# Kernel optimization log

Hardware: AMD Instinct MI355X
Metric: run time of the kernel (lower is better)

Reference implementation:

```python
import jax, jax.numpy as jnp
import numpy as np

B, N, F, D = 32, 1024, 128, 128
SCALE = 0.5


def setup_inputs() -> dict:
    key = jax.random.key(0)
    ks = jax.random.split(key, 8)
    atom_query = jax.random.normal(ks[0], (B, N, F), dtype=jnp.float32)
    # binary validity mask (some atoms padded out), shape [B, N, 1]
    mask = (jax.random.uniform(ks[1], (B, N, 1)) < 0.9).astype(jnp.float32)
    s = 1.0 / np.sqrt(F)
    Wq = jax.random.normal(ks[2], (F, D), dtype=jnp.float32) * s
    Wk = jax.random.normal(ks[3], (F, D), dtype=jnp.float32) * s
    Wv = jax.random.normal(ks[4], (F, D), dtype=jnp.float32) * s
    bq = jnp.zeros((D,), jnp.float32)
    bk = jnp.zeros((D,), jnp.float32)
    bv = jnp.zeros((D,), jnp.float32)
    return {"atom_query": atom_query, "mask": mask,
            "Wq": Wq, "bq": bq, "Wk": Wk, "bk": bk, "Wv": Wv, "bv": bv}


def reference(atom_query, mask, Wq, bq, Wk, bk, Wv, bv):
    # projections
    q = atom_query @ Wq + bq            # [B,N,D]
    k = atom_query @ Wk + bk            # [B,N,D]
    v = atom_query @ Wv + bv            # [B,N,D]
    n = q.shape[1]
    dk = (q.shape[-1] ** (-SCALE)) / n  # python float scalar
    q = q * jnp.float32(dk)
    # pairwise energy [B,N,N]
    energy = jnp.einsum('bqd,bkd->bqk', q, k)
    energy = energy * mask              # mask query rows ([B,N,1] broadcast)
    idx = jnp.arange(n)
    energy = energy.at[:, idx, idx].set(0.0)  # remove self-interaction (diag)
    # aggregate attention per query atom [B,N,1]
    agg = jnp.sum(energy, axis=-1, keepdims=True) * mask
    # euclidean normalize along atom axis (tf.linalg.normalize, axis=1)
    nrm = jnp.sqrt(jnp.sum(agg * agg, axis=1, keepdims=True))
    agg = agg / nrm
    agg = agg + (1.0 - mask) * (-1e9)
    attn = jax.nn.softmax(agg, axis=1)  # softmax over atom (query) axis
    # weighted sum of values -> [B,D]
    context = jnp.sum(mask * (attn * v), axis=1)
    return attn, context
```

## Files before the change

### kernel.cpp

```cpp
#include <hip/hip_runtime.h>

#define B_ 32
#define N_ 1024
#define DK_CONST 8.631674575031098e-05f

typedef unsigned short u16;
typedef __attribute__((ext_vector_type(8))) short short8;
typedef __attribute__((ext_vector_type(4))) float floatx4;

__device__ __forceinline__ u16 f2b(float x) {
    union { float f; unsigned u; } v; v.f = x;
    unsigned u = v.u;
    return (u16)((u + 0x7FFFu + ((u >> 16) & 1u)) >> 16);
}
__device__ __forceinline__ float b2f(u16 h) {
    union { unsigned u; float f; } v; v.u = ((unsigned)h) << 16;
    return v.f;
}

__global__ __launch_bounds__(256) void k1_prep(const float* __restrict__ aq,
                                               const float* __restrict__ Wq,
                                               const float* __restrict__ Wk,
                                               float* __restrict__ colsumPart,
                                               u16* __restrict__ WqT,
                                               u16* __restrict__ WkT) {
    __shared__ float cspart[256][4];
    __shared__ float tr[128][132];
    int t = threadIdx.x;
    int blk = blockIdx.x;
    if (blk < 256) {
        const float4* aq4 = (const float4*)(aq + (size_t)blk * 16384);
        float c0 = 0.f, c1 = 0.f, c2 = 0.f, c3 = 0.f;
        for (int j = 0; j < 16; ++j) {
            float4 v = aq4[t + 256 * j];
            c0 += v.x; c1 += v.y; c2 += v.z; c3 += v.w;
        }
        cspart[t][0] = c0; cspart[t][1] = c1; cspart[t][2] = c2; cspart[t][3] = c3;
        __syncthreads();
        if (t < 128) {
            int c4i = t >> 2, comp = t & 3;
            float s = 0.f;
            for (int h = 0; h < 8; ++h) s += cspart[h * 32 + c4i][comp];
            colsumPart[blk * 128 + t] = s;
        }
    } else {
        const float* W = (blk == 256) ? Wq : Wk;
        u16* WT = (blk == 256) ? WqT : WkT;
        const float4* W4 = (const float4*)W;
        for (int j = 0; j < 16; ++j) {
            int idx = t + 256 * j;
            int f  = idx >> 5;
            int d4 = (idx & 31) * 4;
            float4 v = W4[idx];
            *((float4*)&tr[f][d4]) = v;
        }
        __syncthreads();
        for (int j = 0; j < 16; ++j) {
            int idx = t + 256 * j;
            int d = idx >> 5;
            int c = idx & 31;
            ushort4 o;
            o.x = f2b(tr[4 * c][d]);
            o.y = f2b(tr[4 * c + 1][d]);
            o.z = f2b(tr[4 * c + 2][d]);
            o.w = f2b(tr[4 * c + 3][d]);
            ((ushort4*)WT)[d * 32 + c] = o;
        }
    }
}

__global__ __launch_bounds__(256, 1) void k2_agg(const float* __restrict__ aq,
                                                 const float* __restrict__ mask,
                                                 const float* __restrict__ Wk,
                                                 const float* __restrict__ bq,
                                                 const float* __restrict__ bk,
                                                 const u16* __restrict__ WqT,
                                                 const u16* __restrict__ WkT,
                                                 const float* __restrict__ colsumPart,
                                                 float* __restrict__ agg,
                                                 float* __restrict__ ssqPart) {
    __shared__ __align__(16) u16 aqT[128][136];
    __shared__ __align__(16) u16 wqS[128][136];
    __shared__ __align__(16) u16 wkS[128][136];
    __shared__ float qpart[2][128];
    __shared__ float Ksum_s[128];
    __shared__ float bq_s[128], bk_s[128];
    __shared__ float Ss[128];
    __shared__ float red[256];

    int t = threadIdx.x;
    int tile = blockIdx.x;
    int b = tile >> 3;

    const float4* aq4 = (const float4*)(aq + (size_t)tile * 16384);
    for (int j = 0; j < 16; ++j) {
        int idx = t + 256 * j;
        int row = idx >> 5;
        int c4  = idx & 31;
        float4 v = aq4[idx];
        ushort4 bb;
        bb.x = f2b(v.x); bb.y = f2b(v.y); bb.z = f2b(v.z); bb.w = f2b(v.w);
        *((ushort4*)&aqT[row][c4 * 4]) = bb;
    }
    for (int j = 0; j < 16; ++j) {
        int idx = t + 256 * j;
        int row = idx >> 5;
        int c4  = idx & 31;
        ushort4 q4 = ((const ushort4*)WqT)[idx];
        *((ushort4*)&wqS[row][c4 * 4]) = q4;
        ushort4 k4 = ((const ushort4*)WkT)[idx];
        *((ushort4*)&wkS[row][c4 * 4]) = k4;
    }
    if (t < 128) {
        float s = 0.f;
        for (int h = 0; h < 8; ++h) s += colsumPart[(b * 8 + h) * 128 + t];
        Ss[t] = s;
        bq_s[t] = bq[t];
        bk_s[t] = bk[t];
    }
    __syncthreads();
    if (t < 128) {
        float kd = 1024.0f * bk_s[t];
        for (int f = 0; f < 128; ++f) kd += Ss[f] * Wk[f * 128 + t];
        Ksum_s[t] = kd;
    }
    __syncthreads();

    int w = t >> 6;
    int lane = t & 63;
    int wr   = (w >> 1) * 64;
    int wcol = (w & 1) * 64;
    int lm = lane & 15;
    int lq = lane >> 4;

    floatx4 acc1[4][4], acc2[4][4];
    for (int i = 0; i < 4; ++i)
        for (int j = 0; j < 4; ++j) {
            acc1[i][j] = (floatx4){0.f, 0.f, 0.f, 0.f};
            acc2[i][j] = (floatx4){0.f, 0.f, 0.f, 0.f};
        }

    for (int ks = 0; ks < 4; ++ks) {
        int k0 = ks * 32 + lq * 8;
        short8 afr[4], bq_f[4], bk_f[4];
        for (int i = 0; i < 4; ++i) {
            afr[i]  = *(const short8*)&aqT[wr + i * 16 + lm][k0];
            bq_f[i] = *(const short8*)&wqS[wcol + i * 16 + lm][k0];
            bk_f[i] = *(const short8*)&wkS[wcol + i * 16 + lm][k0];
        }
        for (int i = 0; i < 4; ++i)
            for (int j = 0; j < 4; ++j) {
                acc1[i][j] = __builtin_amdgcn_mfma_f32_16x16x32_bf16(afr[i], bq_f[j], acc1[i][j], 0, 0, 0);
                acc2[i][j] = __builtin_amdgcn_mfma_f32_16x16x32_bf16(afr[i], bk_f[j], acc2[i][j], 0, 0, 0);
            }
    }

    for (int mi = 0; mi < 4; ++mi) {
        for (int r = 0; r < 4; ++r) {
            int row = wr + mi * 16 + lq * 4 + r;
            float s = 0.f;
            for (int nj = 0; nj < 4; ++nj) {
                int col = wcol + nj * 16 + lm;
                float qv = acc1[mi][nj][r] + bq_s[col];
                float kv = Ksum_s[col] - acc2[mi][nj][r] - bk_s[col];
                s += qv * kv;
            }
            s += __shfl_xor(s, 1);
            s += __shfl_xor(s, 2);
            s += __shfl_xor(s, 4);
            s += __shfl_xor(s, 8);
            if (lm == 0) qpart[w & 1][row] = s;
        }
    }
    __syncthreads();
    float a2 = 0.f;
    if (t < 128) {
        int atom = tile * 128 + t;
        float a = mask[atom] * DK_CONST * (qpart[0][t] + qpart[1][t]);
        agg[atom] = a;
        a2 = a * a;
    }
    red[t] = a2;
    __syncthreads();
    for (int st = 128; st > 0; st >>= 1) { if (t < st) red[t] += red[t + st]; __syncthreads(); }
    if (t == 0) ssqPart[tile] = red[0];
}

__global__ __launch_bounds__(1024) void k3_fin(const float* __restrict__ aq,
                                               const float* __restrict__ mask,
                                               const float* __restrict__ Wv,
                                               const float* __restrict__ bv,
                                               const float* __restrict__ agg,
                                               const float* __restrict__ ssqPart,
                                               float* __restrict__ attnOut,
                                               float* __restrict__ ctxOut) {
    __shared__ float el[1024];
    __shared__ float red[1024];
    __shared__ float accs[32][128];
    __shared__ float pvec[128];
    __shared__ float sc0;
    int b = blockIdx.x, t = threadIdx.x;

    if (t == 0) {
        float ss = 0.f;
        for (int h = 0; h < 8; ++h) ss += ssqPart[b * 8 + h];
        sc0 = 1.0f / sqrtf(ss);
    }
    __syncthreads();
    float invn = sc0;
    int atom = b * N_ + t;
    float a = agg[atom];
    float m = mask[atom];
    float e = (m > 0.5f) ? expf(a * invn) : 0.f;
    el[t] = e;
    red[t] = e;
    __syncthreads();
    for (int st = 512; st > 0; st >>= 1) {
        if (t < st) red[t] += red[t + st];
        __syncthreads();
    }
    float invE = 1.0f / red[0];
    attnOut[atom] = e * invE;

    int f4 = t & 31, g = t >> 5;
    const float4* aqb4 = (const float4*)(aq + (size_t)b * N_ * 128);
    float4 acc; acc.x = acc.y = acc.z = acc.w = 0.f;
    for (int i = g; i < 1024; i += 32) {
        float4 v = aqb4[i * 32 + f4];
        float wgt = el[i];
        acc.x += wgt * v.x; acc.y += wgt * v.y; acc.z += wgt * v.z; acc.w += wgt * v.w;
    }
    *((float4*)&accs[g][f4 * 4]) = acc;
    __syncthreads();
    if (t < 128) {
        float p = 0.f;
        for (int gg = 0; gg < 32; ++gg) p += accs[gg][t];
        pvec[t] = p;
    }
    __syncthreads();
    if (t < 128) {
        float c = 0.f;
        for (int f = 0; f < 128; ++f) c += pvec[f] * Wv[f * 128 + t];
        ctxOut[b * 128 + t] = c * invE + bv[t];
    }
}

extern "C" void kernel_launch(void* const* d_in, const int* in_sizes, int n_in,
                              void* d_out, int out_size, void* d_ws, size_t ws_size,
                              hipStream_t stream) {
    const float* aq   = (const float*)d_in[0];
    const float* mask = (const float*)d_in[1];
    const float* Wq   = (const float*)d_in[2];
    const float* bq   = (const float*)d_in[3];
    const float* Wk   = (const float*)d_in[4];
    const float* bk   = (const float*)d_in[5];
    const float* Wv   = (const float*)d_in[6];
    const float* bv   = (const float*)d_in[7];

    float* out_attn = (float*)d_out;
    float* out_ctx  = out_attn + B_ * N_;

    float* wsf        = (float*)d_ws;
    float* colsumPart = wsf;
    float* agg        = wsf + 32768;
    float* ssqPart    = wsf + 65536;
    u16*   WqT        = (u16*)(wsf + 65792);
    u16*   WkT        = (u16*)(wsf + 73984);

    k1_prep<<<258, 256, 0, stream>>>(aq, Wq, Wk, colsumPart, WqT, WkT);
    k2_agg<<<256, 256, 0, stream>>>(aq, mask, Wk, bq, bk, WqT, WkT, colsumPart, agg, ssqPart);
    k3_fin<<<32, 1024, 0, stream>>>(aq, mask, Wv, bv, agg, ssqPart, out_attn, out_ctx);
}
```

Before: 106.3 us.

## Split final softmax/context kernel across atom slices with atomic context accumulation

The final kernel previously ran one 1024-thread block per batch, so only 32 blocks streamed the 16 MB activation tensor. It now launches 32x8 blocks of 256 threads. Each block recomputes the softmax denominator for its batch, then handles a 128-atom slice and atomically adds its partial context into the output. The output context is zeroed in the prep kernel, and Wv is staged in shared memory. In exchange, each block redundantly computes the exponentials and norm, and float atomics make the summation order nondeterministic.

```diff
diff --git a/kernel.cpp b/kernel.cpp
--- a/kernel.cpp
+++ b/kernel.cpp
@@ -12,10 +12,6 @@
     union { float f; unsigned u; } v; v.f = x;
     unsigned u = v.u;
     return (u16)((u + 0x7FFFu + ((u >> 16) & 1u)) >> 16);
-}
-__device__ __forceinline__ float b2f(u16 h) {
-    union { unsigned u; float f; } v; v.u = ((unsigned)h) << 16;
-    return v.f;
 }
 
 __global__ __launch_bounds__(256) void k1_prep(const float* __restrict__ aq,
@@ -23,7 +19,8 @@
                                                const float* __restrict__ Wk,
                                                float* __restrict__ colsumPart,
                                                u16* __restrict__ WqT,
-                                               u16* __restrict__ WkT) {
+                                               u16* __restrict__ WkT,
+                                               float* __restrict__ ctxOut) {
     __shared__ float cspart[256][4];
     __shared__ float tr[128][132];
     int t = threadIdx.x;
@@ -44,6 +41,9 @@
             colsumPart[blk * 128 + t] = s;
         }
     } else {
+        if (blk == 256) {
+            for (int j = 0; j < 16; ++j) ctxOut[t + 256 * j] = 0.f;
+        }
         const float* W = (blk == 256) ? Wq : Wk;
         u16* WT = (blk == 256) ? WqT : WkT;
         const float4* W4 = (const float4*)W;
@@ -186,62 +186,78 @@
     if (t == 0) ssqPart[tile] = red[0];
 }
 
-__global__ __launch_bounds__(1024) void k3_fin(const float* __restrict__ aq,
-                                               const float* __restrict__ mask,
-                                               const float* __restrict__ Wv,
-                                               const float* __restrict__ bv,
-                                               const float* __restrict__ agg,
-                                               const float* __restrict__ ssqPart,
-                                               float* __restrict__ attnOut,
-                                               float* __restrict__ ctxOut) {
+__global__ __launch_bounds__(256) void k3_fin(const float* __restrict__ aq,
+                                              const float* __restrict__ agg,
+                                              const float* __restrict__ mask,
+                                              const float* __restrict__ Wv,
+                                              const float* __restrict__ bv,
+                                              const float* __restrict__ ssqPart,
+                                              float* __restrict__ attnOut,
+                                              float* __restrict__ ctxOut) {
     __shared__ float el[1024];
-    __shared__ float red[1024];
-    __shared__ float accs[32][128];
+    __shared__ float red[256];
+    __shared__ float accs[8][128];
     __shared__ float pvec[128];
-    __shared__ float sc0;
-    int b = blockIdx.x, t = threadIdx.x;
-
-    if (t == 0) {
-        float ss = 0.f;
-        for (int h = 0; h < 8; ++h) ss += ssqPart[b * 8 + h];
-        sc0 = 1.0f / sqrtf(ss);
-    }
-    __syncthreads();
-    float invn = sc0;
-    int atom = b * N_ + t;
-    float a = agg[atom];
-    float m = mask[atom];
-    float e = (m > 0.5f) ? expf(a * invn) : 0.f;
-    el[t] = e;
-    red[t] = e;
-    __syncthreads();
-    for (int st = 512; st > 0; st >>= 1) {
+    __shared__ __align__(16) float wv[128][128];
+    int b = blockIdx.x, s = blockIdx.y, t = threadIdx.x;
+    int base = b * N_;
+
+    float ss = 0.f;
+    for (int h = 0; h < 8; ++h) ss += ssqPart[b * 8 + h];
+    float invn = 1.0f / sqrtf(ss);
+
+    float epart = 0.f;
+    for (int j = 0; j < 4; ++j) {
+        int i = j * 256 + t;
+        float a = agg[base + i];
+        float m = mask[base + i];
+        float e = (m > 0.5f) ? expf(a * invn) : 0.f;
+        el[i] = e;
+        epart += e;
+    }
+    red[t] = epart;
+    __syncthreads();
+    for (int st = 128; st > 0; st >>= 1) {
         if (t < st) red[t] += red[t + st];
         __syncthreads();
     }
     float invE = 1.0f / red[0];
-    attnOut[atom] = e * invE;
-
-    int f4 = t & 31, g = t >> 5;
-    const float4* aqb4 = (const float4*)(aq + (size_t)b * N_ * 128);
-    float4 acc; acc.x = acc.y = acc.z = acc.w = 0.f;
-    for (int i = g; i < 1024; i += 32) {
-        float4 v = aqb4[i * 32 + f4];
-        float wgt = el[i];
-        acc.x += wgt * v.x; acc.y += wgt * v.y; acc.z += wgt * v.z; acc.w += wgt * v.w;
-    }
-    *((float4*)&accs[g][f4 * 4]) = acc;
+
+    if (t < 128) attnOut[base + s * 128 + t] = el[s * 128 + t] * invE;
+
+    {
+        int f4 = t & 31, g = t >> 5;
+        const float4* aqs4 = (const float4*)(aq + ((size_t)base + s * 128) * 128);
+        float4 acc; acc.x = acc.y = acc.z = acc.w = 0.f;
+        for (int r = g; r < 128; r += 8) {
+            float4 v = aqs4[r * 32 + f4];
+            float wgt = el[s * 128 + r];
+            acc.x += wgt * v.x; acc.y += wgt * v.y; acc.z += wgt * v.z; acc.w += wgt * v.w;
+        }
+        *((float4*)&accs[g][f4 * 4]) = acc;
+    }
+    {
+        const float4* wv4 = (const float4*)Wv;
+        for (int j = 0; j < 16; ++j) {
+            int idx = t + 256 * j;
+            int f  = idx >> 5;
+            int d4 = (idx & 31) * 4;
+            *((float4*)&wv[f][d4]) = wv4[idx];
+        }
+    }
     __syncthreads();
     if (t < 128) {
         float p = 0.f;
-        for (int gg = 0; gg < 32; ++gg) p += accs[gg][t];
+        for (int g = 0; g < 8; ++g) p += accs[g][t];
         pvec[t] = p;
     }
     __syncthreads();
     if (t < 128) {
         float c = 0.f;
-        for (int f = 0; f < 128; ++f) c += pvec[f] * Wv[f * 128 + t];
-        ctxOut[b * 128 + t] = c * invE + bv[t];
+        for (int f = 0; f < 128; ++f) c += pvec[f] * wv[f][t];
+        c *= invE;
+        if (s == 0) c += bv[t];
+        atomicAdd(&ctxOut[b * 128 + t], c);
     }
 }
 
@@ -267,7 +283,7 @@
     u16*   WqT        = (u16*)(wsf + 65792);
     u16*   WkT        = (u16*)(wsf + 73984);
 
-    k1_prep<<<258, 256, 0, stream>>>(aq, Wq, Wk, colsumPart, WqT, WkT);
+    k1_prep<<<258, 256, 0, stream>>>(aq, Wq, Wk, colsumPart, WqT, WkT, out_ctx);
     k2_agg<<<256, 256, 0, stream>>>(aq, mask, Wk, bq, bk, WqT, WkT, colsumPart, agg, ssqPart);
-    k3_fin<<<32, 1024, 0, stream>>>(aq, mask, Wv, bv, agg, ssqPart, out_attn, out_ctx);
-}
+    k3_fin<<<dim3(32, 8), 256, 0, stream>>>(aq, agg, mask, Wv, bv, ssqPart, out_attn, out_ctx);
+}
```

Result: faster. 101.8 us (-4.3%).
